# Kernel tuning notes

Measured on AMD Instinct MI355X. Metric: run time of the kernel, lower is better.

## Reference

```python
import jax, jax.numpy as jnp
import numpy as np

B, S, D, H = 2, 2048, 1024, 16
HD = D // H  # 64
ROPE_BASE = 1024.0


def _rope_tables(seq_len, head_dim, dtype=jnp.float32):
    # inv_freq over head_dim//4 frequencies, padded with zeros to head_dim//2
    inv_freq = (1.0 / ROPE_BASE) ** jnp.linspace(0.0, 1.0, head_dim // 4, dtype=dtype)
    inv_freq = jnp.concatenate([inv_freq, jnp.zeros(head_dim // 4, dtype=dtype)])
    pos = jnp.arange(seq_len, dtype=dtype)
    ang = pos[:, None] * inv_freq[None, :]  # [S, HD//2]
    return jnp.sin(ang), jnp.cos(ang)


def _apply_rope(t, sin, cos):
    # t: [B, H, S, HD]; sin/cos: [S, HD//2]
    t1, t2 = jnp.split(t, 2, axis=-1)
    sin = sin[None, None, :, :]
    cos = cos[None, None, :, :]
    return jnp.concatenate([t1 * cos - t2 * sin, t1 * sin + t2 * cos], axis=-1)


def setup_inputs() -> dict:
    key = jax.random.key(0)
    ks = jax.random.split(key, 6)
    std = 0.02
    x = jax.random.normal(ks[0], (B, S, D), dtype=jnp.float32)
    Wq = jax.random.normal(ks[1], (D, D), dtype=jnp.float32) * std
    Wk = jax.random.normal(ks[2], (D, D), dtype=jnp.float32) * std
    Wv = jax.random.normal(ks[3], (D, D), dtype=jnp.float32) * std
    Wo = jax.random.normal(ks[4], (D, D), dtype=jnp.float32) * std
    bo = jnp.zeros((D,), dtype=jnp.float32)
    # causal block mask (standard create_block_mask causal pattern)
    mask = jnp.tril(jnp.ones((S, S), dtype=bool))
    return {"x": x, "Wq": Wq, "Wk": Wk, "Wv": Wv, "Wo": Wo, "bo": bo, "mask": mask}


def reference(x, Wq, Wk, Wv, Wo, bo, mask):
    b, s, d = x.shape
    h, hd = H, d // H
    # torch Linear: y = x @ W.T
    q = (x @ Wq.T).reshape(b, s, h, hd).transpose(0, 2, 1, 3)
    k = (x @ Wk.T).reshape(b, s, h, hd).transpose(0, 2, 1, 3)
    v = (x @ Wv.T).reshape(b, s, h, hd).transpose(0, 2, 1, 3)
    sin, cos = _rope_tables(s, hd, dtype=x.dtype)
    q = _apply_rope(q, sin, cos)
    k = _apply_rope(k, sin, cos)
    scale = 1.0 / jnp.sqrt(jnp.asarray(hd, dtype=x.dtype))
    scores = jnp.einsum('bhqd,bhkd->bhqk', q, k) * scale
    scores = jnp.where(mask[None, None, :, :], scores, -jnp.inf)
    attn = jax.nn.softmax(scores, axis=-1)
    out = jnp.einsum('bhqk,bhkd->bhqd', attn, v)
    out = out.transpose(0, 2, 1, 3).reshape(b, s, d)
    return out @ Wo.T + bo
```

## Files before the change

### kernel.cpp

```cpp
#include <hip/hip_runtime.h>
#include <hip/hip_bf16.h>
#include <stdint.h>

typedef _Float16 f16;
typedef __attribute__((ext_vector_type(8))) _Float16 f16x8;
typedef __attribute__((ext_vector_type(4))) float f32x4;

constexpr int Bb = 2, Ss = 2048, Dd = 1024, Hh = 16, HDim = 64;

#define MFMA16(a, b, c) __builtin_amdgcn_mfma_f32_16x16x32_f16(a, b, c, 0, 0, 0)
#define GLDS(g, l) __builtin_amdgcn_global_load_lds( \
    (const __attribute__((address_space(1))) void*)(g), \
    (__attribute__((address_space(3))) void*)(l), 16, 0, 0)

__global__ void k_cvt5(const float* __restrict__ x,
                       const float* __restrict__ w0, const float* __restrict__ w1,
                       const float* __restrict__ w2, const float* __restrict__ w3,
                       f16* __restrict__ xo, f16* __restrict__ o0, f16* __restrict__ o1,
                       f16* __restrict__ o2, f16* __restrict__ o3,
                       float* __restrict__ sinT, float* __restrict__ cosT) {
    const int z = blockIdx.y;
    if (z == 5) {
        int i = blockIdx.x * blockDim.x + threadIdx.x;
        if (i < 32768) {
            int s = i >> 4, j = i & 15;
            float ang = (float)s * exp2f(-10.0f * (float)j / 15.0f);
            sinT[i] = sinf(ang);
            cosT[i] = cosf(ang);
        }
        return;
    }
    const float* in; f16* out; int n8;
    switch (z) {
        case 0: in = x;  out = xo; n8 = 524288; break;
        case 1: in = w0; out = o0; n8 = 131072; break;
        case 2: in = w1; out = o1; n8 = 131072; break;
        case 3: in = w2; out = o2; n8 = 131072; break;
        default: in = w3; out = o3; n8 = 131072; break;
    }
    for (int i = blockIdx.x * blockDim.x + threadIdx.x; i < n8;
         i += gridDim.x * blockDim.x) {
        float4 a = ((const float4*)in)[2 * i];
        float4 b = ((const float4*)in)[2 * i + 1];
        f16x8 o = {(f16)a.x, (f16)a.y, (f16)a.z, (f16)a.w,
                   (f16)b.x, (f16)b.y, (f16)b.z, (f16)b.w};
        ((f16x8*)out)[i] = o;
    }
}

template <bool FINAL>
__global__ __launch_bounds__(256) void k_gemm(
    const f16* __restrict__ A,
    const f16* __restrict__ B0, const f16* __restrict__ B1, const f16* __restrict__ B2,
    void* C0, void* C1, void* C2,
    const float* __restrict__ bias,
    const float* __restrict__ sinT, const float* __restrict__ cosT,
    int M, int N, int K) {
    __shared__ f16 As[2][128 * 32];
    __shared__ f16 Bs[2][128 * 32];

    const int wg = blockIdx.x;
    int m0, n0, z;
    if constexpr (!FINAL) {
        const int xcd = wg & 7, slot = wg >> 3;
        const int mg = xcd >> 1, ng = xcd & 1;
        const int m = mg * 8 + (slot & 7);
        const int nzi = ng * 12 + (slot >> 3);
        z = nzi >> 3;
        m0 = m * 128; n0 = (nzi & 7) * 128;
    } else {
        const int xcd = wg & 7, slot = wg >> 3;
        const int m = xcd * 4 + (slot & 3);
        z = 0;
        m0 = m * 128; n0 = (slot >> 2) * 128;
    }
    const f16* Bt = (z == 0) ? B0 : (z == 1) ? B1 : B2;
    void* Cout    = (z == 0) ? C0 : (z == 1) ? C1 : C2;

    const int tid = threadIdx.x;
    const int w = tid >> 6, l = tid & 63;
    const int l15 = l & 15, l4 = l >> 4;
    const int wr = w >> 1, wc = w & 1;

    f32x4 acc[4][4] = {};

    const int f0 = tid, row0 = f0 >> 2, cb0 = ((f0 & 3) * 16) ^ ((row0 & 3) << 4);
    const int f1 = 256 + tid, row1 = f1 >> 2, cb1 = ((f1 & 3) * 16) ^ ((row1 & 3) << 4);
    const char* gA0 = (const char*)(A + (size_t)(m0 + row0) * K) + cb0;
    const char* gA1 = (const char*)(A + (size_t)(m0 + row1) * K) + cb1;
    const char* gB0 = (const char*)(Bt + (size_t)(n0 + row0) * K) + cb0;
    const char* gB1 = (const char*)(Bt + (size_t)(n0 + row1) * K) + cb1;
    const int ld0 = (w * 64) * 16, ld1 = (256 + w * 64) * 16;

#define STAGE(kt, buf)                                        \
    do {                                                      \
        GLDS(gA0 + (size_t)(kt) * 2, (char*)As[buf] + ld0);   \
        GLDS(gA1 + (size_t)(kt) * 2, (char*)As[buf] + ld1);   \
        GLDS(gB0 + (size_t)(kt) * 2, (char*)Bs[buf] + ld0);   \
        GLDS(gB1 + (size_t)(kt) * 2, (char*)Bs[buf] + ld1);   \
    } while (0)

    STAGE(0, 0);
    for (int kt = 0; kt < K; kt += 32) {
        const int cur = (kt >> 5) & 1;
        __syncthreads();
        if (kt + 32 < K) STAGE(kt + 32, cur ^ 1);

        f16x8 af[4], bfr[4];
#pragma unroll
        for (int mf = 0; mf < 4; ++mf) {
            int r = wr * 64 + mf * 16 + l15;
            int byo = r * 64 + ((l4 * 16) ^ ((r & 3) << 4));
            af[mf] = *(const f16x8*)((const char*)As[cur] + byo);
        }
#pragma unroll
        for (int nf = 0; nf < 4; ++nf) {
            int r = wc * 64 + nf * 16 + l15;
            int byo = r * 64 + ((l4 * 16) ^ ((r & 3) << 4));
            bfr[nf] = *(const f16x8*)((const char*)Bs[cur] + byo);
        }
#pragma unroll
        for (int mf = 0; mf < 4; ++mf)
#pragma unroll
            for (int nf = 0; nf < 4; ++nf)
                acc[mf][nf] = MFMA16(af[mf], bfr[nf], acc[mf][nf]);
    }
#undef STAGE

    if constexpr (!FINAL) {
        if (z < 2) {
#pragma unroll
            for (int mf = 0; mf < 4; ++mf) {
#pragma unroll
                for (int r = 0; r < 4; ++r) {
                    int row = m0 + wr * 64 + mf * 16 + l4 * 4 + r;
                    int s = row & (Ss - 1);
                    float cs = cosT[(s << 4) + l15];
                    float sn = sinT[(s << 4) + l15];
                    float t1 = acc[mf][0][r], t2 = acc[mf][2][r];
                    acc[mf][0][r] = t1 * cs - t2 * sn;
                    acc[mf][2][r] = t1 * sn + t2 * cs;
                }
            }
        }
    }

#pragma unroll
    for (int mf = 0; mf < 4; ++mf) {
#pragma unroll
        for (int nf = 0; nf < 4; ++nf) {
            int col = n0 + wc * 64 + nf * 16 + l15;
#pragma unroll
            for (int r = 0; r < 4; ++r) {
                int row = m0 + wr * 64 + mf * 16 + l4 * 4 + r;
                float v = acc[mf][nf][r];
                if constexpr (FINAL) {
                    ((float*)Cout)[(size_t)row * N + col] = v + bias[col];
                } else {
                    ((f16*)Cout)[(size_t)row * N + col] = (f16)v;
                }
            }
        }
    }
}

__global__ __launch_bounds__(256) void k_attn(const f16* __restrict__ Q,
                                              const f16* __restrict__ Kk,
                                              const f16* __restrict__ V,
                                              f16* __restrict__ O) {
    __shared__ f16 Ks[64 * 72];
    __shared__ uint32_t Vt32[64 * 36];
    __shared__ f16 Ps[4 * 16 * 72];

    const int tid = threadIdx.x, w = tid >> 6, l = tid & 63;
    const int l15 = l & 15, l4 = l >> 4;
    const int qi = 31 - (int)blockIdx.y;
    const int q0 = qi * 64;
    const int bh = blockIdx.x, b = bh >> 4, h = bh & 15;
    const size_t rowbase = (size_t)b * Ss * Dd + (size_t)h * HDim;
    const f16* kbase = Kk + rowbase;
    const f16* vbase = V + rowbase;

    const int qb = q0 + w * 16;
    f16x8 aq0, aq1;
    {
        const f16* qp = Q + rowbase + (size_t)(qb + l15) * Dd;
        aq0 = *(const f16x8*)(qp + l4 * 8);
        aq1 = *(const f16x8*)(qp + 32 + l4 * 8);
        const f16 c2 = (f16)0.18033688f;
#pragma unroll
        for (int j = 0; j < 8; ++j) { aq0[j] *= c2; aq1[j] *= c2; }
    }

    f32x4 o[4] = {};
    f32x4 osum = {};
    const f16x8 ones = {(f16)1.f, (f16)1.f, (f16)1.f, (f16)1.f,
                        (f16)1.f, (f16)1.f, (f16)1.f, (f16)1.f};

    const int srow = tid >> 2, sc0 = (tid & 3) * 16;
    const int kvp = tid >> 3, dg = tid & 7;
    const int ntiles = qi + 1;
    f16* Pw = Ps + w * (16 * 72);

    f16x8 k8a = *(const f16x8*)(kbase + (size_t)srow * Dd + sc0);
    f16x8 k8b = *(const f16x8*)(kbase + (size_t)srow * Dd + sc0 + 8);
    f16x8 v8a = *(const f16x8*)(vbase + (size_t)(2 * kvp) * Dd + dg * 8);
    f16x8 v8b = *(const f16x8*)(vbase + (size_t)(2 * kvp + 1) * Dd + dg * 8);

    for (int kt = 0; kt < ntiles; ++kt) {
        const int kv0 = kt * 64;
        __syncthreads();
        *(f16x8*)(Ks + srow * 72 + sc0)     = k8a;
        *(f16x8*)(Ks + srow * 72 + sc0 + 8) = k8b;
        {
            union { f16x8 f; uint16_t u[8]; } ua{v8a}, ub{v8b};
            const int csw = kvp ^ ((dg & 3) << 3);
#pragma unroll
            for (int d = 0; d < 8; ++d) {
                uint32_t val = (uint32_t)ua.u[d] | ((uint32_t)ub.u[d] << 16);
                Vt32[(dg * 8 + d) * 36 + csw] = val;
            }
        }
        __syncthreads();

        if (kt + 1 < ntiles) {
            k8a = *(const f16x8*)(kbase + (size_t)(kv0 + 64 + srow) * Dd + sc0);
            k8b = *(const f16x8*)(kbase + (size_t)(kv0 + 64 + srow) * Dd + sc0 + 8);
            v8a = *(const f16x8*)(vbase + (size_t)(kv0 + 64 + 2 * kvp) * Dd + dg * 8);
            v8b = *(const f16x8*)(vbase + (size_t)(kv0 + 64 + 2 * kvp + 1) * Dd + dg * 8);
        }

        f32x4 sf[4] = {};
#pragma unroll
        for (int kvf = 0; kvf < 4; ++kvf) {
            const f16x8 b0 = *(const f16x8*)(Ks + (kvf * 16 + l15) * 72 + l4 * 8);
            const f16x8 b1 = *(const f16x8*)(Ks + (kvf * 16 + l15) * 72 + 32 + l4 * 8);
            sf[kvf] = MFMA16(aq0, b0, sf[kvf]);
            sf[kvf] = MFMA16(aq1, b1, sf[kvf]);
        }

        const int xpw = l4 << 3;
        if (kt + 1 < ntiles) {
#pragma unroll
            for (int kvf = 0; kvf < 4; ++kvf) {
                const int cw = ((8 * kvf + (l15 >> 1)) ^ xpw) * 2 + (l15 & 1);
#pragma unroll
                for (int r = 0; r < 4; ++r)
                    Pw[(l4 * 4 + r) * 72 + cw] =
                        (f16)__builtin_amdgcn_exp2f(sf[kvf][r]);
            }
        } else {
#pragma unroll
            for (int kvf = 0; kvf < 4; ++kvf) {
                const int kv = kv0 + kvf * 16 + l15;
                const int cw = ((8 * kvf + (l15 >> 1)) ^ xpw) * 2 + (l15 & 1);
#pragma unroll
                for (int r = 0; r < 4; ++r) {
                    float p = __builtin_amdgcn_exp2f(sf[kvf][r]);
                    if (kv > qb + l4 * 4 + r) p = 0.f;
                    Pw[(l4 * 4 + r) * 72 + cw] = (f16)p;
                }
            }
        }

        const int xpr = ((l15 >> 2) & 3) << 3;
        const f16x8 pa0 = *(const f16x8*)(Pw + l15 * 72 + ((l4 * 4) ^ xpr) * 2);
        const f16x8 pa1 = *(const f16x8*)(Pw + l15 * 72 + ((l4 * 4 + 16) ^ xpr) * 2);
#pragma unroll
        for (int df = 0; df < 4; ++df) {
            const int xvr = ((2 * df + (l15 >> 3)) & 3) << 3;
            const int rb = (df * 16 + l15) * 36;
            const f16x8 bv0 = *(const f16x8*)(Vt32 + rb + ((l4 * 4) ^ xvr));
            const f16x8 bv1 = *(const f16x8*)(Vt32 + rb + ((l4 * 4 + 16) ^ xvr));
            o[df] = MFMA16(pa0, bv0, o[df]);
            o[df] = MFMA16(pa1, bv1, o[df]);
        }
        osum = MFMA16(pa0, ones, osum);
        osum = MFMA16(pa1, ones, osum);
    }

#pragma unroll
    for (int r = 0; r < 4; ++r) {
        const float inv = 1.0f / osum[r];
        const int qs = qb + l4 * 4 + r;
        f16* op = O + (size_t)(b * Ss + qs) * Dd + h * HDim + l15;
#pragma unroll
        for (int df = 0; df < 4; ++df) op[df * 16] = (f16)(o[df][r] * inv);
    }
}

extern "C" void kernel_launch(void* const* d_in, const int* in_sizes, int n_in,
                              void* d_out, int out_size, void* d_ws, size_t ws_size,
                              hipStream_t stream) {
    const float* x  = (const float*)d_in[0];
    const float* Wq = (const float*)d_in[1];
    const float* Wk = (const float*)d_in[2];
    const float* Wv = (const float*)d_in[3];
    const float* Wo = (const float*)d_in[4];
    const float* bo = (const float*)d_in[5];

    char* ws = (char*)d_ws;
    f16* x16  = (f16*)(ws);
    f16* a16  = (f16*)(ws);
    f16* q16  = (f16*)(ws + (8u << 20));
    f16* k16  = (f16*)(ws + (16u << 20));
    f16* v16  = (f16*)(ws + (24u << 20));
    f16* wq16 = (f16*)(ws + (32u << 20));
    f16* wk16 = (f16*)(ws + (34u << 20));
    f16* wv16 = (f16*)(ws + (36u << 20));
    f16* wo16 = (f16*)(ws + (38u << 20));
    float* sinT = (float*)(ws + (40u << 20));
    float* cosT = (float*)(ws + (40u << 20) + (128u << 10));

    k_cvt5<<<dim3(512, 6), 256, 0, stream>>>(x, Wq, Wk, Wv, Wo,
                                             x16, wq16, wk16, wv16, wo16,
                                             sinT, cosT);

    k_gemm<false><<<768, 256, 0, stream>>>(x16, wq16, wk16, wv16,
                                           (void*)q16, (void*)k16, (void*)v16,
                                           nullptr, sinT, cosT, 4096, 1024, 1024);

    k_attn<<<dim3(32, 32), 256, 0, stream>>>(q16, k16, v16, a16);

    k_gemm<true><<<256, 256, 0, stream>>>(a16, wo16, wo16, wo16,
                                          d_out, d_out, d_out,
                                          bo, nullptr, nullptr, 4096, 1024, 1024);
}
```

Baseline: 115.6 us.

## Split attention waves into 2x2 query/key grid with direct K register loads

The attention kernel now maps its four waves onto a 2x2 grid: each wave handles 32 query rows and a 32-wide half of each KV tile. K fragments are loaded straight from global memory into registers instead of being staged through LDS, and waves whose KV half lies fully above the causal diagonal skip their compute. Partial outputs and row sums from the two key-split waves are combined through shared memory at the end. This is meant to cut wasted work on diagonal tiles and reduce LDS traffic, at the cost of extra reduction syncs, more registers and uncoalesced per-wave K loads.

```diff
diff --git a/kernel.cpp b/kernel.cpp
--- a/kernel.cpp
+++ b/kernel.cpp
@@ -168,50 +168,59 @@
                                               const f16* __restrict__ Kk,
                                               const f16* __restrict__ V,
                                               f16* __restrict__ O) {
-    __shared__ f16 Ks[64 * 72];
-    __shared__ uint32_t Vt32[64 * 36];
-    __shared__ f16 Ps[4 * 16 * 72];
+    __shared__ f16 smem[64 * 72 + 2 * 32 * 72];
+    uint32_t* Vt32 = (uint32_t*)smem;
 
     const int tid = threadIdx.x, w = tid >> 6, l = tid & 63;
     const int l15 = l & 15, l4 = l >> 4;
+    const int wq = w >> 1, wk = w & 1;
     const int qi = 31 - (int)blockIdx.y;
     const int q0 = qi * 64;
     const int bh = blockIdx.x, b = bh >> 4, h = bh & 15;
     const size_t rowbase = (size_t)b * Ss * Dd + (size_t)h * HDim;
     const f16* kbase = Kk + rowbase;
     const f16* vbase = V + rowbase;
-
-    const int qb = q0 + w * 16;
-    f16x8 aq0, aq1;
-    {
-        const f16* qp = Q + rowbase + (size_t)(qb + l15) * Dd;
-        aq0 = *(const f16x8*)(qp + l4 * 8);
-        aq1 = *(const f16x8*)(qp + 32 + l4 * 8);
+    const int qw0 = q0 + wq * 32;
+    f16* Psw = smem + 64 * 72 + wq * (32 * 72);
+
+    f16x8 aq[2][2];
+#pragma unroll
+    for (int m = 0; m < 2; ++m) {
+        const f16* qp = Q + rowbase + (size_t)(qw0 + 16 * m + l15) * Dd;
+        aq[m][0] = *(const f16x8*)(qp + l4 * 8);
+        aq[m][1] = *(const f16x8*)(qp + 32 + l4 * 8);
         const f16 c2 = (f16)0.18033688f;
 #pragma unroll
-        for (int j = 0; j < 8; ++j) { aq0[j] *= c2; aq1[j] *= c2; }
-    }
-
-    f32x4 o[4] = {};
-    f32x4 osum = {};
+        for (int j = 0; j < 8; ++j) { aq[m][0][j] *= c2; aq[m][1][j] *= c2; }
+    }
+
+    f32x4 o[2][4] = {};
+    f32x4 osum[2] = {};
     const f16x8 ones = {(f16)1.f, (f16)1.f, (f16)1.f, (f16)1.f,
                         (f16)1.f, (f16)1.f, (f16)1.f, (f16)1.f};
 
-    const int srow = tid >> 2, sc0 = (tid & 3) * 16;
     const int kvp = tid >> 3, dg = tid & 7;
     const int ntiles = qi + 1;
-    f16* Pw = Ps + w * (16 * 72);
-
-    f16x8 k8a = *(const f16x8*)(kbase + (size_t)srow * Dd + sc0);
-    f16x8 k8b = *(const f16x8*)(kbase + (size_t)srow * Dd + sc0 + 8);
+
     f16x8 v8a = *(const f16x8*)(vbase + (size_t)(2 * kvp) * Dd + dg * 8);
     f16x8 v8b = *(const f16x8*)(vbase + (size_t)(2 * kvp + 1) * Dd + dg * 8);
 
     for (int kt = 0; kt < ntiles; ++kt) {
         const int kv0 = kt * 64;
+        const int kvw0 = kv0 + wk * 32;
+        const bool act = (kvw0 <= qw0 + 31);
+
+        f16x8 bk[2][2];
+        if (act) {
+#pragma unroll
+            for (int kvf = 0; kvf < 2; ++kvf) {
+                const f16* kp = kbase + (size_t)(kvw0 + 16 * kvf + l15) * Dd + l4 * 8;
+                bk[kvf][0] = *(const f16x8*)(kp);
+                bk[kvf][1] = *(const f16x8*)(kp + 32);
+            }
+        }
+
         __syncthreads();
-        *(f16x8*)(Ks + srow * 72 + sc0)     = k8a;
-        *(f16x8*)(Ks + srow * 72 + sc0 + 8) = k8b;
         {
             union { f16x8 f; uint16_t u[8]; } ua{v8a}, ub{v8b};
             const int csw = kvp ^ ((dg & 3) << 3);
@@ -224,68 +233,95 @@
         __syncthreads();
 
         if (kt + 1 < ntiles) {
-            k8a = *(const f16x8*)(kbase + (size_t)(kv0 + 64 + srow) * Dd + sc0);
-            k8b = *(const f16x8*)(kbase + (size_t)(kv0 + 64 + srow) * Dd + sc0 + 8);
             v8a = *(const f16x8*)(vbase + (size_t)(kv0 + 64 + 2 * kvp) * Dd + dg * 8);
             v8b = *(const f16x8*)(vbase + (size_t)(kv0 + 64 + 2 * kvp + 1) * Dd + dg * 8);
         }
 
-        f32x4 sf[4] = {};
-#pragma unroll
-        for (int kvf = 0; kvf < 4; ++kvf) {
-            const f16x8 b0 = *(const f16x8*)(Ks + (kvf * 16 + l15) * 72 + l4 * 8);
-            const f16x8 b1 = *(const f16x8*)(Ks + (kvf * 16 + l15) * 72 + 32 + l4 * 8);
-            sf[kvf] = MFMA16(aq0, b0, sf[kvf]);
-            sf[kvf] = MFMA16(aq1, b1, sf[kvf]);
-        }
-
-        const int xpw = l4 << 3;
-        if (kt + 1 < ntiles) {
-#pragma unroll
-            for (int kvf = 0; kvf < 4; ++kvf) {
-                const int cw = ((8 * kvf + (l15 >> 1)) ^ xpw) * 2 + (l15 & 1);
-#pragma unroll
-                for (int r = 0; r < 4; ++r)
-                    Pw[(l4 * 4 + r) * 72 + cw] =
-                        (f16)__builtin_amdgcn_exp2f(sf[kvf][r]);
-            }
-        } else {
-#pragma unroll
-            for (int kvf = 0; kvf < 4; ++kvf) {
-                const int kv = kv0 + kvf * 16 + l15;
-                const int cw = ((8 * kvf + (l15 >> 1)) ^ xpw) * 2 + (l15 & 1);
-#pragma unroll
-                for (int r = 0; r < 4; ++r) {
-                    float p = __builtin_amdgcn_exp2f(sf[kvf][r]);
-                    if (kv > qb + l4 * 4 + r) p = 0.f;
-                    Pw[(l4 * 4 + r) * 72 + cw] = (f16)p;
-                }
-            }
-        }
-
-        const int xpr = ((l15 >> 2) & 3) << 3;
-        const f16x8 pa0 = *(const f16x8*)(Pw + l15 * 72 + ((l4 * 4) ^ xpr) * 2);
-        const f16x8 pa1 = *(const f16x8*)(Pw + l15 * 72 + ((l4 * 4 + 16) ^ xpr) * 2);
-#pragma unroll
-        for (int df = 0; df < 4; ++df) {
-            const int xvr = ((2 * df + (l15 >> 3)) & 3) << 3;
-            const int rb = (df * 16 + l15) * 36;
-            const f16x8 bv0 = *(const f16x8*)(Vt32 + rb + ((l4 * 4) ^ xvr));
-            const f16x8 bv1 = *(const f16x8*)(Vt32 + rb + ((l4 * 4 + 16) ^ xvr));
-            o[df] = MFMA16(pa0, bv0, o[df]);
-            o[df] = MFMA16(pa1, bv1, o[df]);
-        }
-        osum = MFMA16(pa0, ones, osum);
-        osum = MFMA16(pa1, ones, osum);
-    }
-
-#pragma unroll
-    for (int r = 0; r < 4; ++r) {
-        const float inv = 1.0f / osum[r];
-        const int qs = qb + l4 * 4 + r;
-        f16* op = O + (size_t)(b * Ss + qs) * Dd + h * HDim + l15;
-#pragma unroll
-        for (int df = 0; df < 4; ++df) op[df * 16] = (f16)(o[df][r] * inv);
+        if (act) {
+            f32x4 sf[2][2] = {};
+#pragma unroll
+            for (int kvf = 0; kvf < 2; ++kvf)
+#pragma unroll
+                for (int m = 0; m < 2; ++m) {
+                    sf[m][kvf] = MFMA16(aq[m][0], bk[kvf][0], sf[m][kvf]);
+                    sf[m][kvf] = MFMA16(aq[m][1], bk[kvf][1], sf[m][kvf]);
+                }
+
+            const bool full = (kvw0 + 31 <= qw0);
+#pragma unroll
+            for (int m = 0; m < 2; ++m) {
+                const int qbase = qw0 + 16 * m;
+#pragma unroll
+                for (int kvf = 0; kvf < 2; ++kvf) {
+                    f16* pw = Psw + (16 * m + 4 * l4) * 72 +
+                              (((16 * wk + 8 * kvf + (l15 >> 1)) ^ (l4 << 3)) * 2 +
+                               (l15 & 1));
+                    const int kv = kvw0 + 16 * kvf + l15;
+#pragma unroll
+                    for (int r = 0; r < 4; ++r) {
+                        float p = __builtin_amdgcn_exp2f(sf[m][kvf][r]);
+                        if (!full && kv > qbase + 4 * l4 + r) p = 0.f;
+                        pw[r * 72] = (f16)p;
+                    }
+                }
+            }
+
+#pragma unroll
+            for (int m = 0; m < 2; ++m) {
+                const int row = 16 * m + l15;
+                const int fp = (l15 >> 2) & 3;
+                const f16x8 pa = *(const f16x8*)(
+                    Psw + row * 72 + (((16 * wk + 4 * l4) ^ (fp << 3)) * 2));
+#pragma unroll
+                for (int df = 0; df < 4; ++df) {
+                    const int xvr = ((2 * df + (l15 >> 3)) & 3) << 3;
+                    const int rb = (df * 16 + l15) * 36;
+                    const f16x8 bv = *(const f16x8*)(
+                        Vt32 + rb + ((16 * wk + 4 * l4) ^ xvr));
+                    o[m][df] = MFMA16(pa, bv, o[m][df]);
+                }
+                osum[m] = MFMA16(pa, ones, osum[m]);
+            }
+        }
+    }
+
+    float* scr = (float*)smem;
+    __syncthreads();
+    if (wk == 1) {
+#pragma unroll
+        for (int m = 0; m < 2; ++m)
+#pragma unroll
+            for (int df = 0; df < 4; ++df)
+                *(f32x4*)(scr + (((wq * 64 + l) * 2 + m) * 4 + df) * 4) = o[m][df];
+    }
+    __syncthreads();
+    if (wk == 0) {
+#pragma unroll
+        for (int m = 0; m < 2; ++m)
+#pragma unroll
+            for (int df = 0; df < 4; ++df)
+                o[m][df] += *(const f32x4*)(scr + (((wq * 64 + l) * 2 + m) * 4 + df) * 4);
+    }
+    __syncthreads();
+    if (wk == 1) {
+#pragma unroll
+        for (int m = 0; m < 2; ++m)
+            *(f32x4*)(scr + ((wq * 64 + l) * 2 + m) * 4) = osum[m];
+    }
+    __syncthreads();
+    if (wk == 0) {
+#pragma unroll
+        for (int m = 0; m < 2; ++m) {
+            osum[m] += *(const f32x4*)(scr + ((wq * 64 + l) * 2 + m) * 4);
+#pragma unroll
+            for (int r = 0; r < 4; ++r) {
+                const float inv = 1.0f / osum[m][r];
+                const int qs = qw0 + 16 * m + l4 * 4 + r;
+                f16* op = O + (size_t)(b * Ss + qs) * Dd + h * HDim + l15;
+#pragma unroll
+                for (int df = 0; df < 4; ++df) op[df * 16] = (f16)(o[m][df][r] * inv);
+            }
+        }
     }
 }
 
```

Measured after the change: 123.8 us. 1.07x slower.
